# Kernel optimization log

Measured on AMD Instinct MI355X. Metric: run time of the kernel, lower is better.

Reference implementation:

```python
import jax, jax.numpy as jnp
import numpy as np

DIM = 2048
NUM_EXPERTS = 8
N_TOKENS = 8192
SPARSITY = 0.8  # sparsity_constraint parameter (used only to derive static k)
K = max(1, int(SPARSITY * NUM_EXPERTS))  # = 6


def setup_inputs() -> dict:
    key = jax.random.key(0)
    ks = jax.random.split(key, 5)
    scale = 1.0 / np.sqrt(DIM)
    x = jax.random.normal(ks[0], (N_TOKENS, DIM), dtype=jnp.float32)
    Wg = jax.random.uniform(ks[1], (NUM_EXPERTS, DIM), jnp.float32, -scale, scale)
    bg = jax.random.uniform(ks[2], (NUM_EXPERTS,), jnp.float32, -scale, scale)
    We = jax.random.uniform(ks[3], (NUM_EXPERTS, DIM, DIM), jnp.float32, -scale, scale)
    be = jax.random.uniform(ks[4], (NUM_EXPERTS, DIM), jnp.float32, -scale, scale)
    return {"x": x, "Wg": Wg, "bg": bg, "We": We, "be": be}


def reference(x, Wg, bg, We, be):
    # gate scores: [N, E]
    gate_scores = x @ Wg.T + bg
    # top-k expert indices per token: [N, K]
    _, topk_idx = jax.lax.top_k(gate_scores, K)
    # mask[n, e] = expert e is among token n's top-k: [N, E]
    mask = jnp.any(topk_idx[:, :, None] == jnp.arange(NUM_EXPERTS)[None, None, :], axis=1)
    # all expert outputs: [N, E, D]  (We is [E, out, in]; Linear = x @ W.T + b)
    expert_out = jnp.einsum('nd,efd->nef', x, We) + be[None, :, :]
    # combine: unweighted sum of selected experts' outputs (no gate weighting in source)
    out = jnp.sum(expert_out * mask[:, :, None].astype(x.dtype), axis=1)
    return out
```

## Files before the change

kernel.cpp:

```cpp
#include <hip/hip_runtime.h>
#include <hip/hip_bf16.h>
#include <stdint.h>

#define DIM 2048
#define NEXP 8
#define NTOK 8192
#define KSEL 6
#define NPAIR 28
#define SLOTS 92

typedef short bf16x8 __attribute__((ext_vector_type(8)));
typedef unsigned short u16x8 __attribute__((ext_vector_type(8)));
typedef float f32x4 __attribute__((ext_vector_type(4)));
typedef const __attribute__((address_space(1))) unsigned int GU32;
typedef __attribute__((address_space(3))) unsigned int LU32;

static constexpr int PA[NPAIR] = {0,0,0,0,0,0,0,1,1,1,1,1,1,2,2,2,2,2,3,3,3,3,4,4,4,5,5,6};
static constexpr int PB[NPAIR] = {1,2,3,4,5,6,7,2,3,4,5,6,7,3,4,5,6,7,4,5,6,7,5,6,7,6,7,7};

__device__ __forceinline__ unsigned short f2b(float f) {
  union { float f; uint32_t u; } v; v.f = f;
  return (unsigned short)((v.u + 0x7fffu + ((v.u >> 16) & 1u)) >> 16);
}

__global__ __launch_bounds__(256) void gate_kernel(
    const float* __restrict__ x, const float* __restrict__ Wg,
    const float* __restrict__ bg, unsigned short* __restrict__ xB,
    int* __restrict__ pid) {
  int t = threadIdx.x;
  int w = t >> 6, l = t & 63;
  int n = blockIdx.x * 4 + w;
  const float* xr = x + (size_t)n * DIM;
  float xv[32];
#pragma unroll
  for (int j = 0; j < 8; ++j) {
    float4 v = *(const float4*)(xr + 4 * l + 256 * j);
    xv[4 * j + 0] = v.x; xv[4 * j + 1] = v.y;
    xv[4 * j + 2] = v.z; xv[4 * j + 3] = v.w;
  }
  unsigned short* xbr = xB + (size_t)n * DIM;
#pragma unroll
  for (int j = 0; j < 8; ++j) {
    ushort4 o;
    o.x = f2b(xv[4 * j + 0]); o.y = f2b(xv[4 * j + 1]);
    o.z = f2b(xv[4 * j + 2]); o.w = f2b(xv[4 * j + 3]);
    *(ushort4*)(xbr + 4 * l + 256 * j) = o;
  }
  float sc[NEXP];
#pragma unroll
  for (int e = 0; e < NEXP; ++e) {
    const float* wr = Wg + e * DIM;
    float s = 0.f;
#pragma unroll
    for (int j = 0; j < 8; ++j) {
      float4 v = *(const float4*)(wr + 4 * l + 256 * j);
      s += xv[4 * j + 0] * v.x + xv[4 * j + 1] * v.y +
           xv[4 * j + 2] * v.z + xv[4 * j + 3] * v.w;
    }
#pragma unroll
    for (int off = 32; off > 0; off >>= 1) s += __shfl_xor(s, off, 64);
    sc[e] = s + bg[e];
  }
  if (l == 0) {
    int ex0 = -1, ex1 = -1;
#pragma unroll
    for (int e = 0; e < NEXP; ++e) {
      int rank = 0;
#pragma unroll
      for (int j = 0; j < NEXP; ++j)
        rank += (sc[j] > sc[e]) || (sc[j] == sc[e] && j < e);
      if (rank >= KSEL) { if (ex0 < 0) ex0 = e; else if (ex1 < 0) ex1 = e; }
    }
    pid[n] = ex0 * (15 - ex0) / 2 + (ex1 - ex0 - 1);
  }
}

__global__ __launch_bounds__(1024) void bucket_all(
    const int* __restrict__ pid, int* __restrict__ cnt,
    int* __restrict__ tileBase, int* __restrict__ list) {
  __shared__ int lcnt[NPAIR];
  __shared__ int lpos[NPAIR];
  __shared__ int lbase[NPAIR];
  int t = threadIdx.x;
  if (t < NPAIR) { lcnt[t] = 0; lpos[t] = 0; }
  __syncthreads();
  int p[8];
#pragma unroll
  for (int j = 0; j < 8; ++j) {
    p[j] = pid[t + 1024 * j];
    atomicAdd(&lcnt[p[j]], 1);
  }
  __syncthreads();
  if (t == 0) {
    int s = 0, ts = 0;
    for (int q = 0; q < NPAIR; ++q) {
      lbase[q] = s; s += lcnt[q];
      cnt[q] = lcnt[q];
      tileBase[q] = ts; ts += (lcnt[q] + 127) >> 7;
    }
    tileBase[NPAIR] = ts;
  }
  __syncthreads();
#pragma unroll
  for (int j = 0; j < 8; ++j) {
    int pos = atomicAdd(&lpos[p[j]], 1);
    list[p[j] * NTOK + lbase[p[j]] + pos - lbase[p[j]] + 0] = 0;
  }
}

__global__ __launch_bounds__(1024) void bucket_all2(
    const int* __restrict__ pid, int* __restrict__ cnt,
    int* __restrict__ tileBase, int* __restrict__ list) {
  __shared__ int lcnt[NPAIR];
  __shared__ int lpos[NPAIR];
  int t = threadIdx.x;
  if (t < NPAIR) { lcnt[t] = 0; lpos[t] = 0; }
  __syncthreads();
  int p[8];
#pragma unroll
  for (int j = 0; j < 8; ++j) {
    p[j] = pid[t + 1024 * j];
    atomicAdd(&lcnt[p[j]], 1);
  }
  __syncthreads();
  if (t == 0) {
    int ts = 0;
    for (int q = 0; q < NPAIR; ++q) {
      cnt[q] = lcnt[q];
      tileBase[q] = ts; ts += (lcnt[q] + 127) >> 7;
    }
    tileBase[NPAIR] = ts;
  }
  __syncthreads();
#pragma unroll
  for (int j = 0; j < 8; ++j) {
    int pos = atomicAdd(&lpos[p[j]], 1);
    list[p[j] * NTOK + pos] = t + 1024 * j;
  }
}

__global__ __launch_bounds__(256) void biaspair_kernel(
    const float* __restrict__ be, float* __restrict__ biasPair) {
  int f = blockIdx.x * 256 + threadIdx.x;
  float v[NEXP]; float s = 0.f;
#pragma unroll
  for (int e = 0; e < NEXP; ++e) { v[e] = be[e * DIM + f]; s += v[e]; }
#pragma unroll
  for (int pp = 0; pp < NPAIR; ++pp)
    biasPair[pp * DIM + f] = s - v[PA[pp]] - v[PB[pp]];
}

__global__ __launch_bounds__(256) void pairw_kernel(
    const float* __restrict__ We, unsigned short* __restrict__ Wp,
    int fbase, int frows) {
  size_t pos = ((size_t)blockIdx.x * 256 + threadIdx.x) * 8;
  size_t src = (size_t)fbase * DIM + pos;
  float v[NEXP][8];
  float s[8];
#pragma unroll
  for (int i = 0; i < 8; ++i) s[i] = 0.f;
#pragma unroll
  for (int e = 0; e < NEXP; ++e) {
    float4 v0 = *(const float4*)(We + (size_t)e * DIM * DIM + src);
    float4 v1 = *(const float4*)(We + (size_t)e * DIM * DIM + src + 4);
    v[e][0] = v0.x; v[e][1] = v0.y; v[e][2] = v0.z; v[e][3] = v0.w;
    v[e][4] = v1.x; v[e][5] = v1.y; v[e][6] = v1.z; v[e][7] = v1.w;
#pragma unroll
    for (int i = 0; i < 8; ++i) s[i] += v[e][i];
  }
  size_t chunk = (size_t)frows * DIM;
#pragma unroll
  for (int pp = 0; pp < NPAIR; ++pp) {
    int a = PA[pp], b = PB[pp];
    u16x8 o;
#pragma unroll
    for (int i = 0; i < 8; ++i) o[i] = f2b(s[i] - v[a][i] - v[b][i]);
    *(u16x8*)(Wp + (size_t)pp * chunk + pos) = o;
  }
}

__global__ __launch_bounds__(256, 4) void gemm_pair(
    const unsigned short* __restrict__ A, const unsigned short* __restrict__ Wp,
    const int* __restrict__ cnt, const int* __restrict__ list,
    const int* __restrict__ tileBase, const float* __restrict__ biasPair,
    float* __restrict__ out, int fbase, int frows) {
  __shared__ unsigned short sA[128 * 64];
  __shared__ unsigned short sB[128 * 64];
  __shared__ int sRows[128];
  int total = tileBase[NPAIR];
  if (blockIdx.y >= total) return;
  int slot = total - 1 - blockIdx.y;
  int ft = blockIdx.x;
  int p = 0;
  while (p + 1 < NPAIR && tileBase[p + 1] <= slot) ++p;
  int c = cnt[p];
  int m0 = (slot - tileBase[p]) * 128;

  int t = threadIdx.x;
  int w = t >> 6, l = t & 63;
  int wm = w & 1, wn = w >> 1;
  int quad = l >> 4, lr = l & 15;
  int cs = (l & 7) ^ ((l >> 3) & 7);

  if (t < 128) {
    int idx = m0 + t;
    if (idx >= c) idx = c - 1;
    sRows[t] = list[p * NTOK + idx];
  }
  __syncthreads();

  size_t rowOffA[4], rowOffB[4];
#pragma unroll
  for (int i = 0; i < 4; ++i)
    rowOffA[i] = (size_t)sRows[i * 32 + w * 8 + (l >> 3)] * DIM;
  const unsigned short* Bb =
      Wp + (size_t)p * frows * DIM + (size_t)ft * 128 * DIM;
#pragma unroll
  for (int i = 0; i < 4; ++i)
    rowOffB[i] = (size_t)(i * 32 + w * 8 + (l >> 3)) * DIM;

  f32x4 acc[4][4];
#pragma unroll
  for (int mi = 0; mi < 4; ++mi)
#pragma unroll
    for (int ni = 0; ni < 4; ++ni) {
      acc[mi][ni][0] = 0.f; acc[mi][ni][1] = 0.f;
      acc[mi][ni][2] = 0.f; acc[mi][ni][3] = 0.f;
    }

  for (int k0 = 0; k0 < DIM; k0 += 64) {
#pragma unroll
    for (int i = 0; i < 4; ++i) {
      __builtin_amdgcn_global_load_lds((GU32*)(A + rowOffA[i] + k0 + cs * 8),
          (LU32*)(sA + (i * 32 + w * 8) * 64), 16, 0, 0);
      __builtin_amdgcn_global_load_lds((GU32*)(Bb + rowOffB[i] + k0 + cs * 8),
          (LU32*)(sB + (i * 32 + w * 8) * 64), 16, 0, 0);
    }
    __syncthreads();
#pragma unroll
    for (int ks = 0; ks < 2; ++ks) {
      bf16x8 aF[4], bF[4];
#pragma unroll
      for (int mi = 0; mi < 4; ++mi)
        aF[mi] = *(const bf16x8*)(sA + (wm * 64 + mi * 16 + lr) * 64 +
                                  (((ks << 2) | quad) ^ (lr & 7)) * 8);
#pragma unroll
      for (int ni = 0; ni < 4; ++ni)
        bF[ni] = *(const bf16x8*)(sB + (wn * 64 + ni * 16 + lr) * 64 +
                                  (((ks << 2) | quad) ^ (lr & 7)) * 8);
#pragma unroll
      for (int mi = 0; mi < 4; ++mi)
#pragma unroll
        for (int ni = 0; ni < 4; ++ni)
          acc[mi][ni] = __builtin_amdgcn_mfma_f32_16x16x32_bf16(aF[mi], bF[ni], acc[mi][ni], 0, 0, 0);
    }
    __syncthreads();
  }

  int f0 = fbase + ft * 128;
  float bb[4];
#pragma unroll
  for (int ni = 0; ni < 4; ++ni)
    bb[ni] = biasPair[p * DIM + f0 + wn * 64 + ni * 16 + lr];
#pragma unroll
  for (int mi = 0; mi < 4; ++mi) {
#pragma unroll
    for (int i = 0; i < 4; ++i) {
      int lrow = wm * 64 + mi * 16 + quad * 4 + i;
      if (m0 + lrow < c) {
        float* orow = out + (size_t)sRows[lrow] * DIM + f0;
#pragma unroll
        for (int ni = 0; ni < 4; ++ni)
          orow[wn * 64 + ni * 16 + lr] = acc[mi][ni][i] + bb[ni];
      }
    }
  }
}

extern "C" void kernel_launch(void* const* d_in, const int* in_sizes, int n_in,
                              void* d_out, int out_size, void* d_ws, size_t ws_size,
                              hipStream_t stream) {
  const float* x  = (const float*)d_in[0];
  const float* Wg = (const float*)d_in[1];
  const float* bg = (const float*)d_in[2];
  const float* We = (const float*)d_in[3];
  const float* be = (const float*)d_in[4];
  float* out = (float*)d_out;

  char* ws = (char*)d_ws;
  unsigned short* xB = (unsigned short*)ws; ws += (size_t)NTOK * DIM * 2;
  int* pid = (int*)ws;          ws += (size_t)NTOK * 4;
  int* cnt = (int*)ws;          ws += 128;
  int* tileBase = (int*)ws;     ws += 128;
  int* list = (int*)ws;         ws += (size_t)NPAIR * NTOK * 4;
  float* biasPair = (float*)ws; ws += (size_t)NPAIR * DIM * 4;
  unsigned short* Wp = (unsigned short*)ws;

  size_t avail = ws_size - (size_t)(ws - (char*)d_ws);
  int NR = 1;
  while (NR < 16 && (size_t)NPAIR * DIM * (size_t)(DIM / NR) * 2 > avail) NR <<= 1;
  int frows = DIM / NR;

  gate_kernel<<<NTOK / 4, 256, 0, stream>>>(x, Wg, bg, xB, pid);
  bucket_all2<<<1, 1024, 0, stream>>>(pid, cnt, tileBase, list);
  biaspair_kernel<<<DIM / 256, 256, 0, stream>>>(be, biasPair);
  for (int r = 0; r < NR; ++r) {
    int fbase = r * frows;
    pairw_kernel<<<(frows * DIM) / 2048, 256, 0, stream>>>(We, Wp, fbase, frows);
    gemm_pair<<<dim3(frows / 128, SLOTS), 256, 0, stream>>>(
        xB, Wp, cnt, list, tileBase, biasPair, out, fbase, frows);
  }
}
```

Before: 471.5 us.

## Merge bias-pair into bucket kernel, precompute slot tables, split weights in two

Folds the pair-bias computation into a second block of the bucketing kernel, which removes one launch. The bucketing kernel now writes per-slot pair and row-offset tables, so each GEMM block reads its slot directly instead of scanning tileBase, and slots are no longer visited in reverse order. The pair-weight build and GEMM are forced into at least two feature-row chunks, which shrinks the bf16 pair-weight buffer at the cost of an extra pair of launches.

After: 461.7 us. 2.1% less time.

```diff
diff --git a/kernel.cpp b/kernel.cpp
--- a/kernel.cpp
+++ b/kernel.cpp
@@ -75,45 +75,27 @@
   }
 }
 
-__global__ __launch_bounds__(1024) void bucket_all(
-    const int* __restrict__ pid, int* __restrict__ cnt,
-    int* __restrict__ tileBase, int* __restrict__ list) {
+__global__ __launch_bounds__(1024) void bucket_kernel(
+    const int* __restrict__ pid, const float* __restrict__ be,
+    int* __restrict__ cnt, int* __restrict__ meta,
+    int* __restrict__ slotP, int* __restrict__ slotM0,
+    int* __restrict__ list, float* __restrict__ biasPair) {
+  int t = threadIdx.x;
+  if (blockIdx.x == 1) {
+#pragma unroll
+    for (int it = 0; it < 2; ++it) {
+      int f = t + 1024 * it;
+      float v[NEXP]; float s = 0.f;
+#pragma unroll
+      for (int e = 0; e < NEXP; ++e) { v[e] = be[e * DIM + f]; s += v[e]; }
+#pragma unroll
+      for (int pp = 0; pp < NPAIR; ++pp)
+        biasPair[pp * DIM + f] = s - v[PA[pp]] - v[PB[pp]];
+    }
+    return;
+  }
   __shared__ int lcnt[NPAIR];
   __shared__ int lpos[NPAIR];
-  __shared__ int lbase[NPAIR];
-  int t = threadIdx.x;
-  if (t < NPAIR) { lcnt[t] = 0; lpos[t] = 0; }
-  __syncthreads();
-  int p[8];
-#pragma unroll
-  for (int j = 0; j < 8; ++j) {
-    p[j] = pid[t + 1024 * j];
-    atomicAdd(&lcnt[p[j]], 1);
-  }
-  __syncthreads();
-  if (t == 0) {
-    int s = 0, ts = 0;
-    for (int q = 0; q < NPAIR; ++q) {
-      lbase[q] = s; s += lcnt[q];
-      cnt[q] = lcnt[q];
-      tileBase[q] = ts; ts += (lcnt[q] + 127) >> 7;
-    }
-    tileBase[NPAIR] = ts;
-  }
-  __syncthreads();
-#pragma unroll
-  for (int j = 0; j < 8; ++j) {
-    int pos = atomicAdd(&lpos[p[j]], 1);
-    list[p[j] * NTOK + lbase[p[j]] + pos - lbase[p[j]] + 0] = 0;
-  }
-}
-
-__global__ __launch_bounds__(1024) void bucket_all2(
-    const int* __restrict__ pid, int* __restrict__ cnt,
-    int* __restrict__ tileBase, int* __restrict__ list) {
-  __shared__ int lcnt[NPAIR];
-  __shared__ int lpos[NPAIR];
-  int t = threadIdx.x;
   if (t < NPAIR) { lcnt[t] = 0; lpos[t] = 0; }
   __syncthreads();
   int p[8];
@@ -127,9 +109,11 @@
     int ts = 0;
     for (int q = 0; q < NPAIR; ++q) {
       cnt[q] = lcnt[q];
-      tileBase[q] = ts; ts += (lcnt[q] + 127) >> 7;
-    }
-    tileBase[NPAIR] = ts;
+      for (int s0 = 0; s0 < lcnt[q]; s0 += 128) {
+        slotP[ts] = q; slotM0[ts] = s0; ++ts;
+      }
+    }
+    meta[0] = ts;
   }
   __syncthreads();
 #pragma unroll
@@ -137,17 +121,6 @@
     int pos = atomicAdd(&lpos[p[j]], 1);
     list[p[j] * NTOK + pos] = t + 1024 * j;
   }
-}
-
-__global__ __launch_bounds__(256) void biaspair_kernel(
-    const float* __restrict__ be, float* __restrict__ biasPair) {
-  int f = blockIdx.x * 256 + threadIdx.x;
-  float v[NEXP]; float s = 0.f;
-#pragma unroll
-  for (int e = 0; e < NEXP; ++e) { v[e] = be[e * DIM + f]; s += v[e]; }
-#pragma unroll
-  for (int pp = 0; pp < NPAIR; ++pp)
-    biasPair[pp * DIM + f] = s - v[PA[pp]] - v[PB[pp]];
 }
 
 __global__ __launch_bounds__(256) void pairw_kernel(
@@ -182,19 +155,18 @@
 __global__ __launch_bounds__(256, 4) void gemm_pair(
     const unsigned short* __restrict__ A, const unsigned short* __restrict__ Wp,
     const int* __restrict__ cnt, const int* __restrict__ list,
-    const int* __restrict__ tileBase, const float* __restrict__ biasPair,
+    const int* __restrict__ meta, const int* __restrict__ slotP,
+    const int* __restrict__ slotM0, const float* __restrict__ biasPair,
     float* __restrict__ out, int fbase, int frows) {
   __shared__ unsigned short sA[128 * 64];
   __shared__ unsigned short sB[128 * 64];
   __shared__ int sRows[128];
-  int total = tileBase[NPAIR];
-  if (blockIdx.y >= total) return;
-  int slot = total - 1 - blockIdx.y;
+  int slot = blockIdx.y;
+  if (slot >= meta[0]) return;
   int ft = blockIdx.x;
-  int p = 0;
-  while (p + 1 < NPAIR && tileBase[p + 1] <= slot) ++p;
+  int p = slotP[slot];
+  int m0 = slotM0[slot];
   int c = cnt[p];
-  int m0 = (slot - tileBase[p]) * 128;
 
   int t = threadIdx.x;
   int w = t >> 6, l = t & 63;
@@ -291,23 +263,25 @@
   unsigned short* xB = (unsigned short*)ws; ws += (size_t)NTOK * DIM * 2;
   int* pid = (int*)ws;          ws += (size_t)NTOK * 4;
   int* cnt = (int*)ws;          ws += 128;
-  int* tileBase = (int*)ws;     ws += 128;
+  int* meta = (int*)ws;         ws += 128;
+  int* slotP = (int*)ws;        ws += 512;
+  int* slotM0 = (int*)ws;       ws += 512;
   int* list = (int*)ws;         ws += (size_t)NPAIR * NTOK * 4;
   float* biasPair = (float*)ws; ws += (size_t)NPAIR * DIM * 4;
   unsigned short* Wp = (unsigned short*)ws;
 
   size_t avail = ws_size - (size_t)(ws - (char*)d_ws);
-  int NR = 1;
+  int NR = 2;
   while (NR < 16 && (size_t)NPAIR * DIM * (size_t)(DIM / NR) * 2 > avail) NR <<= 1;
   int frows = DIM / NR;
 
   gate_kernel<<<NTOK / 4, 256, 0, stream>>>(x, Wg, bg, xB, pid);
-  bucket_all2<<<1, 1024, 0, stream>>>(pid, cnt, tileBase, list);
-  biaspair_kernel<<<DIM / 256, 256, 0, stream>>>(be, biasPair);
+  bucket_kernel<<<2, 1024, 0, stream>>>(pid, be, cnt, meta, slotP, slotM0,
+                                        list, biasPair);
   for (int r = 0; r < NR; ++r) {
     int fbase = r * frows;
     pairw_kernel<<<(frows * DIM) / 2048, 256, 0, stream>>>(We, Wp, fbase, frows);
     gemm_pair<<<dim3(frows / 128, SLOTS), 256, 0, stream>>>(
-        xB, Wp, cnt, list, tileBase, biasPair, out, fbase, frows);
-  }
-}
+        xB, Wp, cnt, list, meta, slotP, slotM0, biasPair, out, fbase, frows);
+  }
+}
```
